# Kernel optimization log

Hardware: AMD Instinct MI355X
Metric: run time of the kernel (lower is better)

## Reference

```python
import jax, jax.numpy as jnp
import numpy as np

NUM_EMBEDDINGS = 1024
EMBEDDING_DIM = 512
COMMITMENT_COST = 0.25


def setup_inputs() -> dict:
    key = jax.random.key(0)
    k1, k2 = jax.random.split(key)
    inputs = jax.random.normal(k1, (128, 512, EMBEDDING_DIM), dtype=jnp.float32)
    # torch init: uniform_(-1/K, 1/K)
    emb_weight = jax.random.uniform(
        k2, (NUM_EMBEDDINGS, EMBEDDING_DIM), dtype=jnp.float32,
        minval=-1.0 / NUM_EMBEDDINGS, maxval=1.0 / NUM_EMBEDDINGS)
    return {"inputs": inputs, "emb_weight": emb_weight}


def reference(inputs, emb_weight):
    K, D = emb_weight.shape
    flat = inputs.reshape(-1, D)  # [N, D]
    # squared euclidean distances to every code: [N, K]
    distances = (jnp.sum(flat * flat, axis=1, keepdims=True)
                 + jnp.sum(emb_weight * emb_weight, axis=1)
                 - 2.0 * jnp.matmul(flat, emb_weight.T))
    encoding_indices = jnp.argmin(distances, axis=1)  # [N]
    encodings = jax.nn.one_hot(encoding_indices, K, dtype=inputs.dtype)  # [N, K]
    # matmul(one_hot, W) == gather; use gather (same math, efficient form)
    quantized = jnp.take(emb_weight, encoding_indices, axis=0).reshape(inputs.shape)
    e_latent_loss = jnp.mean((jax.lax.stop_gradient(quantized) - inputs) ** 2)
    q_latent_loss = jnp.mean((quantized - jax.lax.stop_gradient(inputs)) ** 2)
    loss = q_latent_loss + COMMITMENT_COST * e_latent_loss
    # straight-through estimator
    quantized_st = inputs + jax.lax.stop_gradient(quantized - inputs)
    avg_probs = jnp.mean(encodings, axis=0)
    perplexity = jnp.exp(-jnp.sum(avg_probs * jnp.log(avg_probs + 1e-10)))
    return (loss, quantized_st, perplexity, encodings)
```

## Files before the change

kernel.cpp:

```cpp
#include <hip/hip_runtime.h>
#include <stdint.h>

typedef unsigned short u16;
typedef unsigned long long u64;
using short8 = __attribute__((ext_vector_type(8))) short;
using f32x16 = __attribute__((ext_vector_type(16))) float;
using f32x4v = __attribute__((ext_vector_type(4))) float;

#define NROWS 65536
#define DIM   512
#define KC    1024

#define GLOBAL_AS __attribute__((address_space(1)))
#define LDS_AS    __attribute__((address_space(3)))

__device__ __forceinline__ void gload_lds16(const void* g, void* l) {
  __builtin_amdgcn_global_load_lds((const GLOBAL_AS uint32_t*)g,
                                   (LDS_AS uint32_t*)l, 16, 0, 0);
}

__device__ __forceinline__ u16 f2bf(float f) {
  unsigned u = __float_as_uint(f);
  return (u16)((u + 0x7fffu + ((u >> 16) & 1u)) >> 16);
}

__device__ __forceinline__ f32x4v ntload4(const float* p) {
  return __builtin_nontemporal_load((const f32x4v*)p);
}
__device__ __forceinline__ void ntstore4(float* p, f32x4v v) {
  __builtin_nontemporal_store(v, (f32x4v*)p);
}

__global__ __launch_bounds__(256) void wprep_kernel(const float* __restrict__ W,
                                                    short8* __restrict__ WhT8,
                                                    float* __restrict__ wnorm,
                                                    int* __restrict__ counts,
                                                    double* __restrict__ sums) {
  if (blockIdx.x == 0) {
    for (int k = threadIdx.x; k < KC; k += 256) counts[k] = 0;
    if (threadIdx.x < 2) sums[threadIdx.x] = 0.0;
  }
  int code = blockIdx.x * 4 + (threadIdx.x >> 6);
  int l = threadIdx.x & 63;
  const float* wr = W + (size_t)code * DIM + l * 8;
  float4 v0 = *(const float4*)wr;
  float4 v1 = *(const float4*)(wr + 4);
  float s = v0.x * v0.x + v0.y * v0.y + v0.z * v0.z + v0.w * v0.w
          + v1.x * v1.x + v1.y * v1.y + v1.z * v1.z + v1.w * v1.w;
  short8 pk;
  pk[0] = (short)f2bf(v0.x); pk[1] = (short)f2bf(v0.y);
  pk[2] = (short)f2bf(v0.z); pk[3] = (short)f2bf(v0.w);
  pk[4] = (short)f2bf(v1.x); pk[5] = (short)f2bf(v1.y);
  pk[6] = (short)f2bf(v1.z); pk[7] = (short)f2bf(v1.w);
  WhT8[(size_t)(code >> 5) * 2048 + (l >> 1) * 64 + (l & 1) * 32 + (code & 31)] = pk;
#pragma unroll
  for (int off = 32; off; off >>= 1) s += __shfl_xor(s, off, 64);
  if (l == 0) wnorm[code] = s;
}

__global__ __launch_bounds__(256)
__attribute__((amdgpu_waves_per_eu(2, 2))) void mm_kernel(
    const float* __restrict__ X, const float* __restrict__ W,
    const u16* __restrict__ WhTf, const float* __restrict__ wnorm,
    int* __restrict__ counts, double* __restrict__ sums,
    float* __restrict__ out, float* __restrict__ encf) {
  __shared__ __align__(16) u16 BsU[2][16384];
  __shared__ int rowk[128];
  __shared__ double sdbl[4];
  const int t = threadIdx.x;
  const int w = t >> 6, l = t & 63;
  const int r = l & 31, h = l >> 5;
  const int row0 = blockIdx.x * 128;

#pragma unroll
  for (int i = 0; i < 8; ++i)
    gload_lds16(WhTf + i * 2048 + t * 8, &BsU[0][i * 2048 + t * 8]);

  const float* Xr = X + (size_t)(row0 + w * 32 + r) * DIM + h * 8;
  short8 aF[32];
  double xacc = 0.0;
#pragma unroll
  for (int s = 0; s < 32; ++s) {
    f32x4v v0 = ntload4(Xr + s * 16);
    f32x4v v1 = ntload4(Xr + s * 16 + 4);
    xacc += (double)v0[0] * v0[0] + (double)v0[1] * v0[1] + (double)v0[2] * v0[2] + (double)v0[3] * v0[3]
          + (double)v1[0] * v1[0] + (double)v1[1] * v1[1] + (double)v1[2] * v1[2] + (double)v1[3] * v1[3];
    short8 pk;
    pk[0] = (short)f2bf(v0[0]); pk[1] = (short)f2bf(v0[1]);
    pk[2] = (short)f2bf(v0[2]); pk[3] = (short)f2bf(v0[3]);
    pk[4] = (short)f2bf(v1[0]); pk[5] = (short)f2bf(v1[1]);
    pk[6] = (short)f2bf(v1[2]); pk[7] = (short)f2bf(v1[3]);
    aF[s] = pk;
  }
#pragma unroll
  for (int off = 32; off; off >>= 1) xacc += __shfl_xor(xacc, off, 64);
  if (l == 0) atomicAdd(&sums[0], xacc);

  unsigned best_[16];
#pragma unroll
  for (int q = 0; q < 16; ++q) best_[q] = 0xFFFFFFFFu;

  f32x4v* encz = (f32x4v*)(encf + (size_t)row0 * KC);
  const f32x4v zero4 = {0.f, 0.f, 0.f, 0.f};

  asm volatile("s_waitcnt vmcnt(0)" ::: "memory");
  __builtin_amdgcn_s_barrier();
  __builtin_amdgcn_sched_barrier(0);

  for (int kt = 0; kt < 32; ++kt) {
    const int buf = kt & 1;
    if (kt < 31) {
      const u16* src = WhTf + (size_t)(kt + 1) * 16384;
#pragma unroll
      for (int i = 0; i < 8; ++i)
        gload_lds16(src + i * 2048 + t * 8, &BsU[buf ^ 1][i * 2048 + t * 8]);
    }
#pragma unroll
    for (int j = 0; j < 4; ++j)
      __builtin_nontemporal_store(zero4, &encz[kt * 1024 + j * 256 + t]);

    const u16* bufp = &BsU[buf][l * 8];
    f32x16 acc_e = {}, acc_o = {};
#pragma unroll
    for (int ks = 0; ks < 32; ++ks) {
      short8 bv = *(const short8*)&bufp[ks * 512];
      if (ks & 1)
        acc_o = __builtin_amdgcn_mfma_f32_32x32x16_bf16(aF[ks], bv, acc_o, 0, 0, 0);
      else
        acc_e = __builtin_amdgcn_mfma_f32_32x32x16_bf16(aF[ks], bv, acc_e, 0, 0, 0);
    }
    float wn = wnorm[kt * 32 + r];
    unsigned col = (unsigned)(kt * 32 + r);
#pragma unroll
    for (int q = 0; q < 16; ++q) {
      float sc = fmaf(-2.0f, acc_e[q] + acc_o[q], wn);
      unsigned u_ = __float_as_uint(sc);
      unsigned key = (u_ & 0x80000000u) ? ~u_ : (u_ | 0x80000000u);
      best_[q] = min(best_[q], (key & 0xFFFFFC00u) | col);
    }
    asm volatile("s_waitcnt vmcnt(4)" ::: "memory");
    __builtin_amdgcn_s_barrier();
    __builtin_amdgcn_sched_barrier(0);
  }

  double local = 0.0;
#pragma unroll
  for (int q = 0; q < 16; ++q) {
    unsigned pb = best_[q];
#pragma unroll
    for (int off = 16; off; off >>= 1)
      pb = min(pb, (unsigned)__shfl_xor((int)pb, off, 32));
    if (r == 0) {
      int rit = w * 32 + (q & 3) + 8 * (q >> 2) + 4 * h;
      int k = (int)(pb & 1023u);
      rowk[rit] = k;
      atomicAdd(&counts[k], 1);
      unsigned key = (pb & 0xFFFFFC00u) | 0x200u;
      unsigned uu = (key & 0x80000000u) ? (key ^ 0x80000000u) : ~key;
      local += (double)__uint_as_float(uu);
    }
  }
  {
    double o32 = __shfl(local, 32, 64);
    if (l == 0) sdbl[w] = local + o32;
  }
  __syncthreads();
  if (t == 0) atomicAdd(&sums[1], sdbl[0] + sdbl[1] + sdbl[2] + sdbl[3]);

  for (int j = 0; j < 32; ++j) {
    int rit = w * 32 + j;
    int k = rowk[rit];
    const float* Wr = W + (size_t)k * DIM;
    size_t ob = (size_t)(row0 + rit) * DIM;
    {
      f32x4v cm = *(const f32x4v*)(Wr + 4 * l);
      f32x4v c1 = *(const f32x4v*)(Wr + 4 * l + 4);
      f32x4v sv = {cm[3], c1[0], c1[1], c1[2]};
      ntstore4(out + ob + 4 + 4 * l, sv);
    }
    if (l <= 62) {
      int m = l + 64;
      f32x4v dm = *(const f32x4v*)(Wr + 4 * m);
      f32x4v d1 = *(const f32x4v*)(Wr + 4 * m + 4);
      f32x4v sv = {dm[3], d1[0], d1[1], d1[2]};
      ntstore4(out + ob + 4 + 4 * m, sv);
    }
    if (l < 3) out[ob + 1 + l] = Wr[l];
    if (l == 3) out[ob + 512] = Wr[511];
    if (l == 4) encf[(size_t)(row0 + rit) * KC + k] = 1.0f;
  }
}

__global__ __launch_bounds__(256) void finalize_kernel(
    const int* __restrict__ counts, const double* __restrict__ sums,
    float* __restrict__ out_loss, float* __restrict__ out_perp) {
  __shared__ float red[4];
  int t = threadIdx.x;
  float h = 0.f;
  for (int k = t; k < KC; k += 256) {
    float p = (float)counts[k] / (float)NROWS;
    h -= p * logf(p + 1e-10f);
  }
#pragma unroll
  for (int off = 32; off; off >>= 1) h += __shfl_xor(h, off, 64);
  if ((t & 63) == 0) red[t >> 6] = h;
  __syncthreads();
  if (t == 0) {
    float H = red[0] + red[1] + red[2] + red[3];
    *out_perp = expf(H);
    double m = (sums[0] + sums[1]) / (double)((long long)NROWS * DIM);
    *out_loss = (float)(1.25 * m);
  }
}

extern "C" void kernel_launch(void* const* d_in, const int* in_sizes, int n_in,
                              void* d_out, int out_size, void* d_ws, size_t ws_size,
                              hipStream_t stream) {
  const float* X = (const float*)d_in[0];
  const float* W = (const float*)d_in[1];
  float* out = (float*)d_out;
  char* ws = (char*)d_ws;

  float* out_loss = out;
  float* out_perp = out + 1 + NROWS * DIM;
  float* encf     = out + 2 + NROWS * DIM;

  short8* WhT8   = (short8*)ws;
  float*  wnorm  = (float*)(ws + (1040u << 10));
  int*    counts = (int*)(ws + (1040u << 10) + 4096);
  double* sums   = (double*)(ws + (1040u << 10) + 8192);

  wprep_kernel<<<KC / 4, 256, 0, stream>>>(W, WhT8, wnorm, counts, sums);
  mm_kernel<<<NROWS / 128, 256, 0, stream>>>(X, W, (const u16*)WhT8, wnorm,
                                             counts, sums, out, encf);
  finalize_kernel<<<1, 256, 0, stream>>>(counts, sums, out_loss, out_perp);
}
```

Baseline: 180.4 us.

## Split quantized-output gather into separate kernel and prefetch B fragments from LDS

Moves the gather of codebook rows into the quantized output, and the one-hot scatter, out of the matmul kernel into a new out_kernel. The chosen indices are passed through a workspace array. This is meant to give the write-heavy tail more parallelism and stop it serialising after each block's MFMA loop. The inner MFMA loop also preloads 8 B fragments from LDS ahead of use, a rolling register prefetch that hides LDS latency. The cost is an extra kernel launch and a global round trip for the indices, plus more register pressure in mm_kernel.

```diff
diff --git a/kernel.cpp b/kernel.cpp
--- a/kernel.cpp
+++ b/kernel.cpp
@@ -60,12 +60,11 @@
 
 __global__ __launch_bounds__(256)
 __attribute__((amdgpu_waves_per_eu(2, 2))) void mm_kernel(
-    const float* __restrict__ X, const float* __restrict__ W,
-    const u16* __restrict__ WhTf, const float* __restrict__ wnorm,
+    const float* __restrict__ X, const u16* __restrict__ WhTf,
+    const float* __restrict__ wnorm, int* __restrict__ best_idx,
     int* __restrict__ counts, double* __restrict__ sums,
-    float* __restrict__ out, float* __restrict__ encf) {
+    float* __restrict__ encf) {
   __shared__ __align__(16) u16 BsU[2][16384];
-  __shared__ int rowk[128];
   __shared__ double sdbl[4];
   const int t = threadIdx.x;
   const int w = t >> 6, l = t & 63;
@@ -120,14 +119,17 @@
       __builtin_nontemporal_store(zero4, &encz[kt * 1024 + j * 256 + t]);
 
     const u16* bufp = &BsU[buf][l * 8];
+    short8 bv[8];
+#pragma unroll
+    for (int i = 0; i < 8; ++i) bv[i] = *(const short8*)&bufp[i * 512];
     f32x16 acc_e = {}, acc_o = {};
 #pragma unroll
     for (int ks = 0; ks < 32; ++ks) {
-      short8 bv = *(const short8*)&bufp[ks * 512];
       if (ks & 1)
-        acc_o = __builtin_amdgcn_mfma_f32_32x32x16_bf16(aF[ks], bv, acc_o, 0, 0, 0);
+        acc_o = __builtin_amdgcn_mfma_f32_32x32x16_bf16(aF[ks], bv[ks & 7], acc_o, 0, 0, 0);
       else
-        acc_e = __builtin_amdgcn_mfma_f32_32x32x16_bf16(aF[ks], bv, acc_e, 0, 0, 0);
+        acc_e = __builtin_amdgcn_mfma_f32_32x32x16_bf16(aF[ks], bv[ks & 7], acc_e, 0, 0, 0);
+      if (ks < 24) bv[ks & 7] = *(const short8*)&bufp[(ks + 8) * 512];
     }
     float wn = wnorm[kt * 32 + r];
     unsigned col = (unsigned)(kt * 32 + r);
@@ -151,9 +153,9 @@
     for (int off = 16; off; off >>= 1)
       pb = min(pb, (unsigned)__shfl_xor((int)pb, off, 32));
     if (r == 0) {
-      int rit = w * 32 + (q & 3) + 8 * (q >> 2) + 4 * h;
+      int row = row0 + w * 32 + (q & 3) + 8 * (q >> 2) + 4 * h;
       int k = (int)(pb & 1023u);
-      rowk[rit] = k;
+      best_idx[row] = k;
       atomicAdd(&counts[k], 1);
       unsigned key = (pb & 0xFFFFFC00u) | 0x200u;
       unsigned uu = (key & 0x80000000u) ? (key ^ 0x80000000u) : ~key;
@@ -166,12 +168,20 @@
   }
   __syncthreads();
   if (t == 0) atomicAdd(&sums[1], sdbl[0] + sdbl[1] + sdbl[2] + sdbl[3]);
-
-  for (int j = 0; j < 32; ++j) {
-    int rit = w * 32 + j;
-    int k = rowk[rit];
+}
+
+__global__ __launch_bounds__(256) void out_kernel(const float* __restrict__ W,
+                                                  const int* __restrict__ best_idx,
+                                                  float* __restrict__ out,
+                                                  float* __restrict__ encf) {
+  const int t = threadIdx.x;
+  const int w = t >> 6, l = t & 63;
+#pragma unroll
+  for (int j = 0; j < 8; ++j) {
+    int rr = blockIdx.x * 32 + w * 8 + j;
+    int k = best_idx[rr];
     const float* Wr = W + (size_t)k * DIM;
-    size_t ob = (size_t)(row0 + rit) * DIM;
+    size_t ob = (size_t)rr * DIM;
     {
       f32x4v cm = *(const f32x4v*)(Wr + 4 * l);
       f32x4v c1 = *(const f32x4v*)(Wr + 4 * l + 4);
@@ -187,7 +197,7 @@
     }
     if (l < 3) out[ob + 1 + l] = Wr[l];
     if (l == 3) out[ob + 512] = Wr[511];
-    if (l == 4) encf[(size_t)(row0 + rit) * KC + k] = 1.0f;
+    if (l == 4) encf[(size_t)rr * KC + k] = 1.0f;
   }
 }
 
@@ -225,13 +235,15 @@
   float* out_perp = out + 1 + NROWS * DIM;
   float* encf     = out + 2 + NROWS * DIM;
 
-  short8* WhT8   = (short8*)ws;
-  float*  wnorm  = (float*)(ws + (1040u << 10));
-  int*    counts = (int*)(ws + (1040u << 10) + 4096);
-  double* sums   = (double*)(ws + (1040u << 10) + 8192);
+  short8* WhT8    = (short8*)ws;
+  float*  wnorm   = (float*)(ws + (1040u << 10));
+  int*    counts  = (int*)(ws + (1040u << 10) + 4096);
+  double* sums    = (double*)(ws + (1040u << 10) + 8192);
+  int*    best_idx= (int*)(ws + (1040u << 10) + 12288);
 
   wprep_kernel<<<KC / 4, 256, 0, stream>>>(W, WhT8, wnorm, counts, sums);
-  mm_kernel<<<NROWS / 128, 256, 0, stream>>>(X, W, (const u16*)WhT8, wnorm,
-                                             counts, sums, out, encf);
+  mm_kernel<<<NROWS / 128, 256, 0, stream>>>(X, (const u16*)WhT8, wnorm,
+                                             best_idx, counts, sums, encf);
+  out_kernel<<<NROWS / 32, 256, 0, stream>>>(W, best_idx, out, encf);
   finalize_kernel<<<1, 256, 0, stream>>>(counts, sums, out_loss, out_perp);
 }
```

After: 189.5 us. +5.0%, slower.

## Enlarge block tile to 256 rows and 64-code chunks to reuse B fragments

Applied to the files above, without the earlier changes.

Each wave now holds two 32-row A fragments and multiplies each B fragment read from LDS against both, while each k-iteration stages a 64-code chunk of the codebook (double-buffered 128KB LDS). The goal is to halve the LDS and global traffic per MFMA for the codebook tiles and to halve the number of loop iterations and barriers. The cost is twice as many registers for A fragments and accumulators, one wave per EU occupancy, half as many blocks (256 over the CUs), and less latency hiding.

```diff
diff --git a/kernel.cpp b/kernel.cpp
--- a/kernel.cpp
+++ b/kernel.cpp
@@ -59,46 +59,55 @@
 }
 
 __global__ __launch_bounds__(256)
-__attribute__((amdgpu_waves_per_eu(2, 2))) void mm_kernel(
+__attribute__((amdgpu_waves_per_eu(1, 1))) void mm_kernel(
     const float* __restrict__ X, const float* __restrict__ W,
     const u16* __restrict__ WhTf, const float* __restrict__ wnorm,
     int* __restrict__ counts, double* __restrict__ sums,
     float* __restrict__ out, float* __restrict__ encf) {
-  __shared__ __align__(16) u16 BsU[2][16384];
-  __shared__ int rowk[128];
+  __shared__ __align__(16) u16 BsU[2][32768];
+  __shared__ int rowk[256];
   __shared__ double sdbl[4];
   const int t = threadIdx.x;
   const int w = t >> 6, l = t & 63;
   const int r = l & 31, h = l >> 5;
-  const int row0 = blockIdx.x * 128;
-
-#pragma unroll
-  for (int i = 0; i < 8; ++i)
-    gload_lds16(WhTf + i * 2048 + t * 8, &BsU[0][i * 2048 + t * 8]);
-
-  const float* Xr = X + (size_t)(row0 + w * 32 + r) * DIM + h * 8;
-  short8 aF[32];
+  const int row0 = blockIdx.x * 256;
+
+#pragma unroll
+  for (int i = 0; i < 16; ++i)
+    gload_lds16(WhTf + (i * 256 + t) * 8, &BsU[0][(i * 256 + t) * 8]);
+
+  const float* Xr0 = X + (size_t)(row0 + w * 64 + r) * DIM + h * 8;
+  const float* Xr1 = Xr0 + 32 * DIM;
+  short8 aF0[32], aF1[32];
   double xacc = 0.0;
 #pragma unroll
   for (int s = 0; s < 32; ++s) {
-    f32x4v v0 = ntload4(Xr + s * 16);
-    f32x4v v1 = ntload4(Xr + s * 16 + 4);
+    f32x4v v0 = ntload4(Xr0 + s * 16);
+    f32x4v v1 = ntload4(Xr0 + s * 16 + 4);
+    f32x4v v2 = ntload4(Xr1 + s * 16);
+    f32x4v v3 = ntload4(Xr1 + s * 16 + 4);
     xacc += (double)v0[0] * v0[0] + (double)v0[1] * v0[1] + (double)v0[2] * v0[2] + (double)v0[3] * v0[3]
-          + (double)v1[0] * v1[0] + (double)v1[1] * v1[1] + (double)v1[2] * v1[2] + (double)v1[3] * v1[3];
-    short8 pk;
-    pk[0] = (short)f2bf(v0[0]); pk[1] = (short)f2bf(v0[1]);
-    pk[2] = (short)f2bf(v0[2]); pk[3] = (short)f2bf(v0[3]);
-    pk[4] = (short)f2bf(v1[0]); pk[5] = (short)f2bf(v1[1]);
-    pk[6] = (short)f2bf(v1[2]); pk[7] = (short)f2bf(v1[3]);
-    aF[s] = pk;
+          + (double)v1[0] * v1[0] + (double)v1[1] * v1[1] + (double)v1[2] * v1[2] + (double)v1[3] * v1[3]
+          + (double)v2[0] * v2[0] + (double)v2[1] * v2[1] + (double)v2[2] * v2[2] + (double)v2[3] * v2[3]
+          + (double)v3[0] * v3[0] + (double)v3[1] * v3[1] + (double)v3[2] * v3[2] + (double)v3[3] * v3[3];
+    short8 p0, p1;
+    p0[0] = (short)f2bf(v0[0]); p0[1] = (short)f2bf(v0[1]);
+    p0[2] = (short)f2bf(v0[2]); p0[3] = (short)f2bf(v0[3]);
+    p0[4] = (short)f2bf(v1[0]); p0[5] = (short)f2bf(v1[1]);
+    p0[6] = (short)f2bf(v1[2]); p0[7] = (short)f2bf(v1[3]);
+    p1[0] = (short)f2bf(v2[0]); p1[1] = (short)f2bf(v2[1]);
+    p1[2] = (short)f2bf(v2[2]); p1[3] = (short)f2bf(v2[3]);
+    p1[4] = (short)f2bf(v3[0]); p1[5] = (short)f2bf(v3[1]);
+    p1[6] = (short)f2bf(v3[2]); p1[7] = (short)f2bf(v3[3]);
+    aF0[s] = p0; aF1[s] = p1;
   }
 #pragma unroll
   for (int off = 32; off; off >>= 1) xacc += __shfl_xor(xacc, off, 64);
   if (l == 0) atomicAdd(&sums[0], xacc);
 
-  unsigned best_[16];
-#pragma unroll
-  for (int q = 0; q < 16; ++q) best_[q] = 0xFFFFFFFFu;
+  unsigned best_[32];
+#pragma unroll
+  for (int q = 0; q < 32; ++q) best_[q] = 0xFFFFFFFFu;
 
   f32x4v* encz = (f32x4v*)(encf + (size_t)row0 * KC);
   const f32x4v zero4 = {0.f, 0.f, 0.f, 0.f};
@@ -107,51 +116,61 @@
   __builtin_amdgcn_s_barrier();
   __builtin_amdgcn_sched_barrier(0);
 
-  for (int kt = 0; kt < 32; ++kt) {
+  for (int kt = 0; kt < 16; ++kt) {
     const int buf = kt & 1;
-    if (kt < 31) {
-      const u16* src = WhTf + (size_t)(kt + 1) * 16384;
-#pragma unroll
-      for (int i = 0; i < 8; ++i)
-        gload_lds16(src + i * 2048 + t * 8, &BsU[buf ^ 1][i * 2048 + t * 8]);
-    }
-#pragma unroll
-    for (int j = 0; j < 4; ++j)
-      __builtin_nontemporal_store(zero4, &encz[kt * 1024 + j * 256 + t]);
+    if (kt < 15) {
+      const u16* src = WhTf + (size_t)(kt + 1) * 32768;
+#pragma unroll
+      for (int i = 0; i < 16; ++i)
+        gload_lds16(src + (i * 256 + t) * 8, &BsU[buf ^ 1][(i * 256 + t) * 8]);
+    }
+#pragma unroll
+    for (int i = 0; i < 16; ++i)
+      __builtin_nontemporal_store(zero4, &encz[kt * 4096 + i * 256 + t]);
 
     const u16* bufp = &BsU[buf][l * 8];
-    f32x16 acc_e = {}, acc_o = {};
-#pragma unroll
-    for (int ks = 0; ks < 32; ++ks) {
-      short8 bv = *(const short8*)&bufp[ks * 512];
-      if (ks & 1)
-        acc_o = __builtin_amdgcn_mfma_f32_32x32x16_bf16(aF[ks], bv, acc_o, 0, 0, 0);
-      else
-        acc_e = __builtin_amdgcn_mfma_f32_32x32x16_bf16(aF[ks], bv, acc_e, 0, 0, 0);
-    }
-    float wn = wnorm[kt * 32 + r];
-    unsigned col = (unsigned)(kt * 32 + r);
-#pragma unroll
-    for (int q = 0; q < 16; ++q) {
-      float sc = fmaf(-2.0f, acc_e[q] + acc_o[q], wn);
-      unsigned u_ = __float_as_uint(sc);
-      unsigned key = (u_ & 0x80000000u) ? ~u_ : (u_ | 0x80000000u);
-      best_[q] = min(best_[q], (key & 0xFFFFFC00u) | col);
-    }
-    asm volatile("s_waitcnt vmcnt(4)" ::: "memory");
+#pragma unroll
+    for (int cb = 0; cb < 2; ++cb) {
+      f32x16 a0e = {}, a0o = {}, a1e = {}, a1o = {};
+#pragma unroll
+      for (int ks = 0; ks < 32; ++ks) {
+        short8 bv = *(const short8*)&bufp[cb * 16384 + ks * 512];
+        if (ks & 1) {
+          a0o = __builtin_amdgcn_mfma_f32_32x32x16_bf16(aF0[ks], bv, a0o, 0, 0, 0);
+          a1o = __builtin_amdgcn_mfma_f32_32x32x16_bf16(aF1[ks], bv, a1o, 0, 0, 0);
+        } else {
+          a0e = __builtin_amdgcn_mfma_f32_32x32x16_bf16(aF0[ks], bv, a0e, 0, 0, 0);
+          a1e = __builtin_amdgcn_mfma_f32_32x32x16_bf16(aF1[ks], bv, a1e, 0, 0, 0);
+        }
+      }
+      float wn = wnorm[kt * 64 + cb * 32 + r];
+      unsigned col = (unsigned)(kt * 64 + cb * 32 + r);
+#pragma unroll
+      for (int q = 0; q < 16; ++q) {
+        float s0 = fmaf(-2.0f, a0e[q] + a0o[q], wn);
+        unsigned u0 = __float_as_uint(s0);
+        unsigned k0 = (u0 & 0x80000000u) ? ~u0 : (u0 | 0x80000000u);
+        best_[q] = min(best_[q], (k0 & 0xFFFFFC00u) | col);
+        float s1 = fmaf(-2.0f, a1e[q] + a1o[q], wn);
+        unsigned u1 = __float_as_uint(s1);
+        unsigned k1 = (u1 & 0x80000000u) ? ~u1 : (u1 | 0x80000000u);
+        best_[16 + q] = min(best_[16 + q], (k1 & 0xFFFFFC00u) | col);
+      }
+    }
+    asm volatile("s_waitcnt vmcnt(16)" ::: "memory");
     __builtin_amdgcn_s_barrier();
     __builtin_amdgcn_sched_barrier(0);
   }
 
   double local = 0.0;
 #pragma unroll
-  for (int q = 0; q < 16; ++q) {
+  for (int q = 0; q < 32; ++q) {
     unsigned pb = best_[q];
 #pragma unroll
     for (int off = 16; off; off >>= 1)
       pb = min(pb, (unsigned)__shfl_xor((int)pb, off, 32));
     if (r == 0) {
-      int rit = w * 32 + (q & 3) + 8 * (q >> 2) + 4 * h;
+      int rit = w * 64 + (q >> 4) * 32 + (q & 3) + 8 * ((q >> 2) & 3) + 4 * h;
       int k = (int)(pb & 1023u);
       rowk[rit] = k;
       atomicAdd(&counts[k], 1);
@@ -167,8 +186,8 @@
   __syncthreads();
   if (t == 0) atomicAdd(&sums[1], sdbl[0] + sdbl[1] + sdbl[2] + sdbl[3]);
 
-  for (int j = 0; j < 32; ++j) {
-    int rit = w * 32 + j;
+  for (int j = 0; j < 64; ++j) {
+    int rit = w * 64 + j;
     int k = rowk[rit];
     const float* Wr = W + (size_t)k * DIM;
     size_t ob = (size_t)(row0 + rit) * DIM;
@@ -231,7 +250,7 @@
   double* sums   = (double*)(ws + (1040u << 10) + 8192);
 
   wprep_kernel<<<KC / 4, 256, 0, stream>>>(W, WhT8, wnorm, counts, sums);
-  mm_kernel<<<NROWS / 128, 256, 0, stream>>>(X, W, (const u16*)WhT8, wnorm,
+  mm_kernel<<<NROWS / 256, 256, 0, stream>>>(X, W, (const u16*)WhT8, wnorm,
                                              counts, sums, out, encf);
   finalize_kernel<<<1, 256, 0, stream>>>(counts, sums, out_loss, out_perp);
 }
```

Result: slower. 248.2 us (+37.6%).

## Split codebook tiles into half-K stages with a 4-deep LDS prefetch ring

Applied to the files above, without the earlier changes.

Changes the codebook LDS pipeline from two 32 KB double buffers to a four-slot ring of 16 KB half-K tiles, prefetching two stages ahead. The wprep layout is reorganised so each 32-code group splits into two contiguous K halves. The goal is more in-flight global-to-LDS loads and finer-grained barriers, so load latency is better hidden behind the MFMA work. In exchange there are twice as many barriers per code group, and the vmcnt accounting has to match the interleaved encoding-zero stores. The last iterations also issue redundant loads of tile 63.

```diff
diff --git a/kernel.cpp b/kernel.cpp
--- a/kernel.cpp
+++ b/kernel.cpp
@@ -52,7 +52,8 @@
   pk[2] = (short)f2bf(v0.z); pk[3] = (short)f2bf(v0.w);
   pk[4] = (short)f2bf(v1.x); pk[5] = (short)f2bf(v1.y);
   pk[6] = (short)f2bf(v1.z); pk[7] = (short)f2bf(v1.w);
-  WhT8[(size_t)(code >> 5) * 2048 + (l >> 1) * 64 + (l & 1) * 32 + (code & 31)] = pk;
+  WhT8[(size_t)(code >> 5) * 2048 + (size_t)(l >> 5) * 1024 +
+       (size_t)((l >> 1) & 15) * 64 + (l & 1) * 32 + (code & 31)] = pk;
 #pragma unroll
   for (int off = 32; off; off >>= 1) s += __shfl_xor(s, off, 64);
   if (l == 0) wnorm[code] = s;
@@ -64,7 +65,7 @@
     const u16* __restrict__ WhTf, const float* __restrict__ wnorm,
     int* __restrict__ counts, double* __restrict__ sums,
     float* __restrict__ out, float* __restrict__ encf) {
-  __shared__ __align__(16) u16 BsU[2][16384];
+  __shared__ __align__(16) u16 BsU[4][8192];
   __shared__ int rowk[128];
   __shared__ double sdbl[4];
   const int t = threadIdx.x;
@@ -73,8 +74,11 @@
   const int row0 = blockIdx.x * 128;
 
 #pragma unroll
-  for (int i = 0; i < 8; ++i)
-    gload_lds16(WhTf + i * 2048 + t * 8, &BsU[0][i * 2048 + t * 8]);
+  for (int pt = 0; pt < 3; ++pt)
+#pragma unroll
+    for (int i = 0; i < 4; ++i)
+      gload_lds16(WhTf + (size_t)pt * 8192 + (i * 256 + t) * 8,
+                  &BsU[pt][(i * 256 + t) * 8]);
 
   const float* Xr = X + (size_t)(row0 + w * 32 + r) * DIM + h * 8;
   short8 aF[32];
@@ -107,40 +111,47 @@
   __builtin_amdgcn_s_barrier();
   __builtin_amdgcn_sched_barrier(0);
 
-  for (int kt = 0; kt < 32; ++kt) {
-    const int buf = kt & 1;
-    if (kt < 31) {
-      const u16* src = WhTf + (size_t)(kt + 1) * 16384;
-#pragma unroll
-      for (int i = 0; i < 8; ++i)
-        gload_lds16(src + i * 2048 + t * 8, &BsU[buf ^ 1][i * 2048 + t * 8]);
-    }
-#pragma unroll
-    for (int j = 0; j < 4; ++j)
-      __builtin_nontemporal_store(zero4, &encz[kt * 1024 + j * 256 + t]);
-
-    const u16* bufp = &BsU[buf][l * 8];
+  for (int cg = 0; cg < 32; ++cg) {
     f32x16 acc_e = {}, acc_o = {};
 #pragma unroll
-    for (int ks = 0; ks < 32; ++ks) {
-      short8 bv = *(const short8*)&bufp[ks * 512];
-      if (ks & 1)
-        acc_o = __builtin_amdgcn_mfma_f32_32x32x16_bf16(aF[ks], bv, acc_o, 0, 0, 0);
-      else
-        acc_e = __builtin_amdgcn_mfma_f32_32x32x16_bf16(aF[ks], bv, acc_e, 0, 0, 0);
-    }
-    float wn = wnorm[kt * 32 + r];
-    unsigned col = (unsigned)(kt * 32 + r);
-#pragma unroll
-    for (int q = 0; q < 16; ++q) {
-      float sc = fmaf(-2.0f, acc_e[q] + acc_o[q], wn);
-      unsigned u_ = __float_as_uint(sc);
-      unsigned key = (u_ & 0x80000000u) ? ~u_ : (u_ | 0x80000000u);
-      best_[q] = min(best_[q], (key & 0xFFFFFC00u) | col);
-    }
-    asm volatile("s_waitcnt vmcnt(4)" ::: "memory");
-    __builtin_amdgcn_s_barrier();
-    __builtin_amdgcn_sched_barrier(0);
+    for (int khalf = 0; khalf < 2; ++khalf) {
+      const int kt = cg * 2 + khalf;
+      {
+        const int nt = (kt + 2 < 64) ? kt + 2 : 63;
+        const u16* src = WhTf + (size_t)nt * 8192;
+#pragma unroll
+        for (int i = 0; i < 4; ++i)
+          gload_lds16(src + (i * 256 + t) * 8,
+                      &BsU[(kt + 2) & 3][(i * 256 + t) * 8]);
+      }
+#pragma unroll
+      for (int j = 0; j < 2; ++j)
+        __builtin_nontemporal_store(zero4, &encz[kt * 512 + j * 256 + t]);
+
+      const u16* bufp = &BsU[kt & 3][l * 8];
+#pragma unroll
+      for (int ks = 0; ks < 16; ++ks) {
+        short8 bv = *(const short8*)&bufp[ks * 512];
+        if (ks & 1)
+          acc_o = __builtin_amdgcn_mfma_f32_32x32x16_bf16(aF[khalf * 16 + ks], bv, acc_o, 0, 0, 0);
+        else
+          acc_e = __builtin_amdgcn_mfma_f32_32x32x16_bf16(aF[khalf * 16 + ks], bv, acc_e, 0, 0, 0);
+      }
+      if (khalf) {
+        float wn = wnorm[cg * 32 + r];
+        unsigned col = (unsigned)(cg * 32 + r);
+#pragma unroll
+        for (int q = 0; q < 16; ++q) {
+          float sc = fmaf(-2.0f, acc_e[q] + acc_o[q], wn);
+          unsigned u_ = __float_as_uint(sc);
+          unsigned key = (u_ & 0x80000000u) ? ~u_ : (u_ | 0x80000000u);
+          best_[q] = min(best_[q], (key & 0xFFFFFC00u) | col);
+        }
+      }
+      asm volatile("s_waitcnt vmcnt(6)" ::: "memory");
+      __builtin_amdgcn_s_barrier();
+      __builtin_amdgcn_sched_barrier(0);
+    }
   }
 
   double local = 0.0;
```

Result: slower. 188.0 us (+4.3%).
